# Kernel tuning notes

Measured on AMD Instinct MI355X. Metric: run time of the kernel, lower is better.

Reference implementation:

```python
import jax, jax.numpy as jnp
import numpy as np

GT_MASK_LEN = 128   # processor_dct.gt_mask_len
N_KEEP = 256        # processor_dct.n_keep


def _zigzag_flat_positions(n):
    """Row-major flat index of the k-th element in JPEG zigzag order of an n x n grid."""
    order = []
    for s in range(2 * n - 1):
        if s % 2 == 0:  # even diagonals traverse up-right
            for i in range(min(s, n - 1), max(-1, s - n), -1):
                order.append((i, s - i))
        else:
            for j in range(min(s, n - 1), max(-1, s - n), -1):
                order.append((s - j, j))
    return np.array([i * n + j for (i, j) in order], dtype=np.int64)


def _dct_matrix(n):
    """Orthonormal DCT-II matrix C (cv2.dct). cv2.idct(Y) == C.T @ Y @ C in 2-D."""
    k = np.arange(n)[:, None].astype(np.float64)
    m = np.arange(n)[None, :].astype(np.float64)
    C = np.sqrt(2.0 / n) * np.cos(np.pi * (2 * m + 1) * k / (2 * n))
    C[0, :] = np.sqrt(1.0 / n)
    return C.astype(np.float32)

_ZZ_POS = jnp.asarray(_zigzag_flat_positions(GT_MASK_LEN)[:N_KEEP])
_DCT_C = jnp.asarray(_dct_matrix(GT_MASK_LEN))


def setup_inputs() -> dict:
    key = jax.random.key(0)
    k1, k2, k3, k4 = jax.random.split(key, 4)
    B, R, C = 8, 300, 91
    pred_logits = jax.random.normal(k1, (B, R, C), dtype=jnp.float32)
    pred_boxes = jax.random.uniform(k2, (B, R, 4), dtype=jnp.float32) * 0.5 + 0.25
    pred_vectors = jax.random.normal(k3, (B, R, N_KEEP), dtype=jnp.float32)
    target_sizes = jax.random.randint(k4, (B, 2), 512, 1334, dtype=jnp.int32)
    return {"pred_logits": pred_logits, "pred_boxes": pred_boxes,
            "pred_vectors": pred_vectors, "target_sizes": target_sizes}


def reference(pred_logits, pred_boxes, pred_vectors, target_sizes):
    L = GT_MASK_LEN
    # --- classification scores ---
    prob = jax.nn.sigmoid(pred_logits)            # [B,R,C]
    scores = prob.max(axis=2)                     # [B,R]
    labels = prob.argmax(axis=2)                  # [B,R] int
    # --- boxes: cxcywh -> xyxy, rescale to image size ---
    cx, cy, w, h = jnp.split(pred_boxes, 4, axis=-1)
    boxes = jnp.concatenate([cx - 0.5 * w, cy - 0.5 * h,
                             cx + 0.5 * w, cy + 0.5 * h], axis=-1)  # [B,R,4]
    ts = target_sizes.astype(jnp.float32)
    img_h, img_w = ts[:, 0], ts[:, 1]
    scale_fct = jnp.stack([img_w, img_h, img_w, img_h], axis=1)     # [B,4]
    boxes = boxes * scale_fct[:, None, :]
    # --- masks: inverse zigzag scatter + batched separable 2-D IDCT ---
    B, R, _ = pred_vectors.shape
    flat = jnp.zeros((B, R, L * L), dtype=pred_vectors.dtype)
    flat = flat.at[:, :, _ZZ_POS].set(pred_vectors)
    coef = flat.reshape(B, R, L, L)
    # cv2.idct(Y) = C^T Y C (orthonormal DCT-III)
    re_mask = jnp.einsum('iu,bruv,vj->brij', _DCT_C.T, coef, _DCT_C)  # [B,R,L,L]
    max_v = re_mask.max(axis=(-2, -1), keepdims=True)
    min_v = re_mask.min(axis=(-2, -1), keepdims=True)
    masks = jnp.where(re_mask > (max_v + min_v) * 0.5, 1.0, 0.0).astype(jnp.float32)
    return scores, labels, boxes, masks
```

## Files before the change

### kernel.cpp

```cpp
#include <hip/hip_runtime.h>
#include <math.h>

#define NROWS 2400
#define NCLS  91
#define L     128
#define KSUB  23
#define NKEEP 256

#define TAB_OFF  2944
#define M1_OFF   2944
#define COEF_OFF 5888
#define RED_OFF  6440
#define SMEM_FLOATS 6448

__global__ void __launch_bounds__(256)
postproc_kernel(const float* __restrict__ logits,
                const float* __restrict__ pboxes,
                const float* __restrict__ vecs,
                const int*   __restrict__ tsz,
                float* __restrict__ out)
{
    __shared__ float smem[SMEM_FLOATS];
    const int br  = blockIdx.x;
    const int tid = threadIdx.x;

    if (tid < 64) {
        const float* lrow = logits + (size_t)br * NCLS;
        float p = 1.0f / (1.0f + expf(-lrow[tid]));
        int   bi = tid;
        if (tid < NCLS - 64) {
            float p2 = 1.0f / (1.0f + expf(-lrow[tid + 64]));
            if (p2 > p) { p = p2; bi = tid + 64; }
        }
        #pragma unroll
        for (int off = 32; off > 0; off >>= 1) {
            float po = __shfl_xor(p, off, 64);
            int   io = __shfl_xor(bi, off, 64);
            if (po > p || (po == p && io < bi)) { p = po; bi = io; }
        }
        if (tid == 0) {
            out[br] = p;
            out[NROWS + br] = (float)bi;
            const int b = br / 300;
            const float W = (float)tsz[2 * b + 1];
            const float H = (float)tsz[2 * b + 0];
            const float4 bx = *(const float4*)(pboxes + (size_t)br * 4);
            float4 o;
            o.x = (bx.x - 0.5f * bx.z) * W;
            o.y = (bx.y - 0.5f * bx.w) * H;
            o.z = (bx.x + 0.5f * bx.z) * W;
            o.w = (bx.y + 0.5f * bx.w) * H;
            *(float4*)(out + 2 * NROWS + (size_t)br * 4) = o;
        }
    }

    double* tab = (double*)&smem[TAB_OFF];
    for (int t = tid; t < 512; t += 256)
        tab[t] = cos((3.14159265358979323846 / 256.0) * (double)t);
    __syncthreads();

    {
        const double s0 = sqrt(1.0 / 128.0);
        for (int idx = tid; idx < KSUB * L; idx += 256) {
            const int u = idx >> 7, m = idx & 127;
            float v;
            if (u == 0) v = (float)s0;
            else        v = (float)(0.125 * tab[((2 * m + 1) * u) & 511]);
            smem[idx] = v;
        }
    }
    float* coef = &smem[COEF_OFF];
    for (int t = tid; t < KSUB * 24; t += 256) {
        const int u = t / 24, v = t - u * 24;
        const int s = u + v;
        if (v == 23 || s > 22 || (s == 22 && u < 20)) coef[t] = 0.0f;
    }
    {
        const int k = tid;
        int s = 0;
        while ((s + 1) * (s + 2) / 2 <= k) ++s;
        const int r = k - s * (s + 1) / 2;
        const int u  = (s & 1) ? r : (s - r);
        const int vv = (s & 1) ? (s - r) : r;
        coef[u * 24 + vv] = vecs[(size_t)br * NKEEP + k];
    }
    __syncthreads();

    float* M1 = &smem[M1_OFF];
    {
        const int i = tid & 127;
        float cs[KSUB];
        #pragma unroll
        for (int u = 0; u < KSUB; ++u) cs[u] = smem[u * L + i];

        if (tid < 128) {
            float a[12];
            #pragma unroll
            for (int v = 0; v < 12; ++v) a[v] = 0.0f;
            #pragma unroll
            for (int u = 0; u < KSUB; ++u) {
                const float4 c0 = *(const float4*)&coef[u * 24 + 0];
                const float4 c1 = *(const float4*)&coef[u * 24 + 4];
                const float4 c2 = *(const float4*)&coef[u * 24 + 8];
                const float cu = cs[u];
                a[0]  += cu * c0.x; a[1]  += cu * c0.y; a[2]  += cu * c0.z; a[3]  += cu * c0.w;
                a[4]  += cu * c1.x; a[5]  += cu * c1.y; a[6]  += cu * c1.z; a[7]  += cu * c1.w;
                a[8]  += cu * c2.x; a[9]  += cu * c2.y; a[10] += cu * c2.z; a[11] += cu * c2.w;
            }
            #pragma unroll
            for (int v = 0; v < 12; ++v) M1[v * L + i] = a[v];
        } else {
            float a[11];
            #pragma unroll
            for (int v = 0; v < 11; ++v) a[v] = 0.0f;
            #pragma unroll
            for (int u = 0; u < KSUB; ++u) {
                const float4 c0 = *(const float4*)&coef[u * 24 + 12];
                const float4 c1 = *(const float4*)&coef[u * 24 + 16];
                const float4 c2 = *(const float4*)&coef[u * 24 + 20];
                const float cu = cs[u];
                a[0] += cu * c0.x; a[1] += cu * c0.y; a[2]  += cu * c0.z; a[3] += cu * c0.w;
                a[4] += cu * c1.x; a[5] += cu * c1.y; a[6]  += cu * c1.z; a[7] += cu * c1.w;
                a[8] += cu * c2.x; a[9] += cu * c2.y; a[10] += cu * c2.z;
            }
            #pragma unroll
            for (int v = 0; v < 11; ++v) M1[(v + 12) * L + i] = a[v];
        }
    }
    __syncthreads();

    const int tx = tid & 31, ty = tid >> 5;
    const int j0 = tx << 2, i0 = ty << 4;
    float acc[16][4];
    #pragma unroll
    for (int r = 0; r < 16; ++r)
        #pragma unroll
        for (int q = 0; q < 4; ++q) acc[r][q] = 0.0f;

    for (int v = 0; v < KSUB; ++v) {
        const float4 c = *(const float4*)&smem[v * L + j0];
        #pragma unroll
        for (int g = 0; g < 4; ++g) {
            const float4 m = *(const float4*)&M1[v * L + i0 + 4 * g];
            acc[4*g+0][0] += m.x * c.x; acc[4*g+0][1] += m.x * c.y;
            acc[4*g+0][2] += m.x * c.z; acc[4*g+0][3] += m.x * c.w;
            acc[4*g+1][0] += m.y * c.x; acc[4*g+1][1] += m.y * c.y;
            acc[4*g+1][2] += m.y * c.z; acc[4*g+1][3] += m.y * c.w;
            acc[4*g+2][0] += m.z * c.x; acc[4*g+2][1] += m.z * c.y;
            acc[4*g+2][2] += m.z * c.z; acc[4*g+2][3] += m.z * c.w;
            acc[4*g+3][0] += m.w * c.x; acc[4*g+3][1] += m.w * c.y;
            acc[4*g+3][2] += m.w * c.z; acc[4*g+3][3] += m.w * c.w;
        }
    }

    float mn = acc[0][0], mx = acc[0][0];
    #pragma unroll
    for (int r = 0; r < 16; ++r)
        #pragma unroll
        for (int q = 0; q < 4; ++q) {
            mn = fminf(mn, acc[r][q]);
            mx = fmaxf(mx, acc[r][q]);
        }
    #pragma unroll
    for (int off = 32; off > 0; off >>= 1) {
        mn = fminf(mn, __shfl_xor(mn, off, 64));
        mx = fmaxf(mx, __shfl_xor(mx, off, 64));
    }
    const int w = tid >> 6;
    if ((tid & 63) == 0) { smem[RED_OFF + w] = mn; smem[RED_OFF + 4 + w] = mx; }
    __syncthreads();
    const float gmn = fminf(fminf(smem[RED_OFF + 0], smem[RED_OFF + 1]),
                            fminf(smem[RED_OFF + 2], smem[RED_OFF + 3]));
    const float gmx = fmaxf(fmaxf(smem[RED_OFF + 4], smem[RED_OFF + 5]),
                            fmaxf(smem[RED_OFF + 6], smem[RED_OFF + 7]));
    const float thr = (gmx + gmn) * 0.5f;

    float* omask = out + 6 * NROWS + (size_t)br * (L * L);
    #pragma unroll
    for (int r = 0; r < 16; ++r) {
        float4 o;
        o.x = acc[r][0] > thr ? 1.0f : 0.0f;
        o.y = acc[r][1] > thr ? 1.0f : 0.0f;
        o.z = acc[r][2] > thr ? 1.0f : 0.0f;
        o.w = acc[r][3] > thr ? 1.0f : 0.0f;
        *(float4*)&omask[(i0 + r) * L + j0] = o;
    }
}

extern "C" void kernel_launch(void* const* d_in, const int* in_sizes, int n_in,
                              void* d_out, int out_size, void* d_ws, size_t ws_size,
                              hipStream_t stream)
{
    const float* logits = (const float*)d_in[0];
    const float* pboxes = (const float*)d_in[1];
    const float* vecs   = (const float*)d_in[2];
    const int*   tsz    = (const int*)d_in[3];
    float* out = (float*)d_out;
    (void)d_ws; (void)ws_size; (void)in_sizes; (void)n_in; (void)out_size;

    postproc_kernel<<<dim3(NROWS), dim3(256), 0, stream>>>(logits, pboxes, vecs, tsz, out);
}
```

Measured before the change: 191.0 us.

## Use 512 threads per block and halve per-thread IDCT work

Doubles the block size to 512 threads. Each thread now computes an 8x4 output tile instead of 16x4, and the first-pass DCT columns are split four ways instead of two. The block-level min/max reduction grows to 8 waves. The goal is more wavefronts and lower register pressure, which helps hide latency in this store-bound mask kernel, at the cost of more threads doing per-thread setup and a wider reduction.

```diff
diff --git a/kernel.cpp b/kernel.cpp
--- a/kernel.cpp
+++ b/kernel.cpp
@@ -11,9 +11,9 @@
 #define M1_OFF   2944
 #define COEF_OFF 5888
 #define RED_OFF  6440
-#define SMEM_FLOATS 6448
-
-__global__ void __launch_bounds__(256)
+#define SMEM_FLOATS 6456
+
+__global__ void __launch_bounds__(512, 6)
 postproc_kernel(const float* __restrict__ logits,
                 const float* __restrict__ pboxes,
                 const float* __restrict__ vecs,
@@ -55,13 +55,12 @@
     }
 
     double* tab = (double*)&smem[TAB_OFF];
-    for (int t = tid; t < 512; t += 256)
-        tab[t] = cos((3.14159265358979323846 / 256.0) * (double)t);
+    if (tid < 512) tab[tid] = cos((3.14159265358979323846 / 256.0) * (double)tid);
     __syncthreads();
 
     {
         const double s0 = sqrt(1.0 / 128.0);
-        for (int idx = tid; idx < KSUB * L; idx += 256) {
+        for (int idx = tid; idx < KSUB * L; idx += 512) {
             const int u = idx >> 7, m = idx & 127;
             float v;
             if (u == 0) v = (float)s0;
@@ -70,12 +69,12 @@
         }
     }
     float* coef = &smem[COEF_OFF];
-    for (int t = tid; t < KSUB * 24; t += 256) {
+    for (int t = tid; t < KSUB * 24; t += 512) {
         const int u = t / 24, v = t - u * 24;
         const int s = u + v;
         if (v == 23 || s > 22 || (s == 22 && u < 20)) coef[t] = 0.0f;
     }
-    {
+    if (tid < NKEEP) {
         const int k = tid;
         int s = 0;
         while ((s + 1) * (s + 2) / 2 <= k) ++s;
@@ -89,58 +88,57 @@
     float* M1 = &smem[M1_OFF];
     {
         const int i = tid & 127;
+        const int g = tid >> 7;
         float cs[KSUB];
         #pragma unroll
         for (int u = 0; u < KSUB; ++u) cs[u] = smem[u * L + i];
 
-        if (tid < 128) {
-            float a[12];
-            #pragma unroll
-            for (int v = 0; v < 12; ++v) a[v] = 0.0f;
+        const int vbase = g * 6;
+        float a[6];
+        #pragma unroll
+        for (int v = 0; v < 6; ++v) a[v] = 0.0f;
+        if (g < 3) {
             #pragma unroll
             for (int u = 0; u < KSUB; ++u) {
-                const float4 c0 = *(const float4*)&coef[u * 24 + 0];
-                const float4 c1 = *(const float4*)&coef[u * 24 + 4];
-                const float4 c2 = *(const float4*)&coef[u * 24 + 8];
+                const float2 c0 = *(const float2*)&coef[u * 24 + vbase + 0];
+                const float2 c1 = *(const float2*)&coef[u * 24 + vbase + 2];
+                const float2 c2 = *(const float2*)&coef[u * 24 + vbase + 4];
                 const float cu = cs[u];
-                a[0]  += cu * c0.x; a[1]  += cu * c0.y; a[2]  += cu * c0.z; a[3]  += cu * c0.w;
-                a[4]  += cu * c1.x; a[5]  += cu * c1.y; a[6]  += cu * c1.z; a[7]  += cu * c1.w;
-                a[8]  += cu * c2.x; a[9]  += cu * c2.y; a[10] += cu * c2.z; a[11] += cu * c2.w;
+                a[0] += cu * c0.x; a[1] += cu * c0.y;
+                a[2] += cu * c1.x; a[3] += cu * c1.y;
+                a[4] += cu * c2.x; a[5] += cu * c2.y;
             }
             #pragma unroll
-            for (int v = 0; v < 12; ++v) M1[v * L + i] = a[v];
+            for (int v = 0; v < 6; ++v) M1[(vbase + v) * L + i] = a[v];
         } else {
-            float a[11];
-            #pragma unroll
-            for (int v = 0; v < 11; ++v) a[v] = 0.0f;
             #pragma unroll
             for (int u = 0; u < KSUB; ++u) {
-                const float4 c0 = *(const float4*)&coef[u * 24 + 12];
-                const float4 c1 = *(const float4*)&coef[u * 24 + 16];
-                const float4 c2 = *(const float4*)&coef[u * 24 + 20];
+                const float2 c0 = *(const float2*)&coef[u * 24 + 18];
+                const float2 c1 = *(const float2*)&coef[u * 24 + 20];
+                const float  c2 = coef[u * 24 + 22];
                 const float cu = cs[u];
-                a[0] += cu * c0.x; a[1] += cu * c0.y; a[2]  += cu * c0.z; a[3] += cu * c0.w;
-                a[4] += cu * c1.x; a[5] += cu * c1.y; a[6]  += cu * c1.z; a[7] += cu * c1.w;
-                a[8] += cu * c2.x; a[9] += cu * c2.y; a[10] += cu * c2.z;
+                a[0] += cu * c0.x; a[1] += cu * c0.y;
+                a[2] += cu * c1.x; a[3] += cu * c1.y;
+                a[4] += cu * c2;
             }
             #pragma unroll
-            for (int v = 0; v < 11; ++v) M1[(v + 12) * L + i] = a[v];
-        }
-    }
-    __syncthreads();
-
-    const int tx = tid & 31, ty = tid >> 5;
-    const int j0 = tx << 2, i0 = ty << 4;
-    float acc[16][4];
-    #pragma unroll
-    for (int r = 0; r < 16; ++r)
+            for (int v = 0; v < 5; ++v) M1[(18 + v) * L + i] = a[v];
+        }
+    }
+    __syncthreads();
+
+    const int tx = tid & 31, iy = tid >> 5;
+    const int j0 = tx << 2, i0 = iy << 3;
+    float acc[8][4];
+    #pragma unroll
+    for (int r = 0; r < 8; ++r)
         #pragma unroll
         for (int q = 0; q < 4; ++q) acc[r][q] = 0.0f;
 
     for (int v = 0; v < KSUB; ++v) {
         const float4 c = *(const float4*)&smem[v * L + j0];
         #pragma unroll
-        for (int g = 0; g < 4; ++g) {
+        for (int g = 0; g < 2; ++g) {
             const float4 m = *(const float4*)&M1[v * L + i0 + 4 * g];
             acc[4*g+0][0] += m.x * c.x; acc[4*g+0][1] += m.x * c.y;
             acc[4*g+0][2] += m.x * c.z; acc[4*g+0][3] += m.x * c.w;
@@ -155,7 +153,7 @@
 
     float mn = acc[0][0], mx = acc[0][0];
     #pragma unroll
-    for (int r = 0; r < 16; ++r)
+    for (int r = 0; r < 8; ++r)
         #pragma unroll
         for (int q = 0; q < 4; ++q) {
             mn = fminf(mn, acc[r][q]);
@@ -167,17 +165,19 @@
         mx = fmaxf(mx, __shfl_xor(mx, off, 64));
     }
     const int w = tid >> 6;
-    if ((tid & 63) == 0) { smem[RED_OFF + w] = mn; smem[RED_OFF + 4 + w] = mx; }
-    __syncthreads();
-    const float gmn = fminf(fminf(smem[RED_OFF + 0], smem[RED_OFF + 1]),
-                            fminf(smem[RED_OFF + 2], smem[RED_OFF + 3]));
-    const float gmx = fmaxf(fmaxf(smem[RED_OFF + 4], smem[RED_OFF + 5]),
-                            fmaxf(smem[RED_OFF + 6], smem[RED_OFF + 7]));
+    if ((tid & 63) == 0) { smem[RED_OFF + w] = mn; smem[RED_OFF + 8 + w] = mx; }
+    __syncthreads();
+    float gmn = smem[RED_OFF + 0], gmx = smem[RED_OFF + 8];
+    #pragma unroll
+    for (int k = 1; k < 8; ++k) {
+        gmn = fminf(gmn, smem[RED_OFF + k]);
+        gmx = fmaxf(gmx, smem[RED_OFF + 8 + k]);
+    }
     const float thr = (gmx + gmn) * 0.5f;
 
     float* omask = out + 6 * NROWS + (size_t)br * (L * L);
     #pragma unroll
-    for (int r = 0; r < 16; ++r) {
+    for (int r = 0; r < 8; ++r) {
         float4 o;
         o.x = acc[r][0] > thr ? 1.0f : 0.0f;
         o.y = acc[r][1] > thr ? 1.0f : 0.0f;
@@ -198,5 +198,5 @@
     float* out = (float*)d_out;
     (void)d_ws; (void)ws_size; (void)in_sizes; (void)n_in; (void)out_size;
 
-    postproc_kernel<<<dim3(NROWS), dim3(256), 0, stream>>>(logits, pboxes, vecs, tsz, out);
+    postproc_kernel<<<dim3(NROWS), dim3(512), 0, stream>>>(logits, pboxes, vecs, tsz, out);
 }
```

Result: faster. 187.1 us (-2.0%).
